# Performance work log

Measured on AMD Instinct MI355X. Metric: run time of the kernel, lower is better.

## Reference

```python
import jax, jax.numpy as jnp
import numpy as np

N = 100000   # total nodes in batched graph
E = 320000   # total edges
B = 128      # number of graphs in batch
D_IN = 128
H = 256
OUT = 10
L = 4        # num_layers - 1 conv layers
EPS = 1e-6


def setup_inputs() -> dict:
    key = jax.random.key(0)
    ks = jax.random.split(key, 8)
    h = jax.random.normal(ks[0], (N, D_IN), dtype=jnp.float32)
    src = jax.random.randint(ks[1], (E,), 0, N)
    dst = jax.random.randint(ks[2], (E,), 0, N)
    batch_ids = jnp.sort(jax.random.randint(ks[3], (N,), 0, B))
    s = 0.05
    W_first = jax.random.normal(ks[4], (D_IN, H), dtype=jnp.float32) * s
    b_first = jnp.zeros((H,), jnp.float32)
    W_rest = jax.random.normal(ks[5], (L - 1, H, H), dtype=jnp.float32) * s
    b_rest = jnp.zeros((L - 1, H), jnp.float32)
    gamma = jnp.ones((L, H), jnp.float32)
    beta = jnp.zeros((L, H), jnp.float32)
    mean_scale = jnp.ones((L, H), jnp.float32)
    W_pred = jax.random.normal(ks[6], (H, OUT), dtype=jnp.float32) * s
    b_pred = jnp.zeros((OUT,), jnp.float32)
    return dict(h=h, src=src, dst=dst, batch_ids=batch_ids,
                W_first=W_first, b_first=b_first, W_rest=W_rest, b_rest=b_rest,
                gamma=gamma, beta=beta, mean_scale=mean_scale,
                W_pred=W_pred, b_pred=b_pred)


def _graph_conv(h, W, b, src, dst, dinv_src, dinv_dst):
    # DGL GraphConv, norm='both': D_dst^{-1/2} A D_src^{-1/2} h W + b
    x = h * dinv_src[:, None]
    m = jax.ops.segment_sum(x[src], dst, num_segments=N)
    m = m * dinv_dst[:, None]
    return m @ W + b


def _graph_norm(h, gamma, beta, ms, batch_ids, counts):
    # GraphNorm: per-graph mean (scaled by learnable mean_scale) and std
    mean = jax.ops.segment_sum(h, batch_ids, num_segments=B) / counts[:, None]
    sub = h - mean[batch_ids] * ms
    var = jax.ops.segment_sum(sub * sub, batch_ids, num_segments=B) / counts[:, None]
    inv_std = jax.lax.rsqrt(var + EPS)
    return gamma * sub * inv_std[batch_ids] + beta


def reference(h, src, dst, batch_ids, W_first, b_first, W_rest, b_rest,
              gamma, beta, mean_scale, W_pred, b_pred):
    ones_e = jnp.ones((E,), h.dtype)
    deg_out = jnp.maximum(jax.ops.segment_sum(ones_e, src, num_segments=N), 1.0)
    deg_in = jnp.maximum(jax.ops.segment_sum(ones_e, dst, num_segments=N), 1.0)
    dinv_src = jax.lax.rsqrt(deg_out)
    dinv_dst = jax.lax.rsqrt(deg_in)
    counts = jnp.maximum(
        jax.ops.segment_sum(jnp.ones((N,), h.dtype), batch_ids, num_segments=B), 1.0)

    for i in range(L):
        x = h
        if i == 0:
            h = _graph_conv(h, W_first, b_first, src, dst, dinv_src, dinv_dst)
        else:
            h = _graph_conv(h, W_rest[i - 1], b_rest[i - 1], src, dst, dinv_src, dinv_dst)
        h = _graph_norm(h, gamma[i], beta[i], mean_scale[i], batch_ids, counts)
        if i != 0:
            h = jax.nn.relu(h) + x
        else:
            h = jax.nn.relu(h)

    pooled = jax.ops.segment_sum(h, batch_ids, num_segments=B)  # [B, H]
    # dropout is identity at eval
    return pooled @ W_pred + b_pred
```

## Files before the change

### kernel.cpp

```cpp
#include <hip/hip_runtime.h>

#define N_NODES 100000
#define N_PAD   100096
#define N_EDGES 320000
#define NB      128
#define DIN     128
#define H       256
#define OUT_DIM 10
#define EPSV    1e-6f
#define SCAN_B  256
#define PSLICES 32
#define NBLK    (N_PAD / 64)
#define NXCD    8

typedef unsigned short bf16_t;
typedef __attribute__((ext_vector_type(8))) short bf16x8;
typedef __attribute__((ext_vector_type(4))) float f32x4;

__device__ __forceinline__ float bf2f(bf16_t u) {
    union { unsigned int i; float f; } x;
    x.i = ((unsigned int)u) << 16;
    return x.f;
}
__device__ __forceinline__ bf16_t f2bf(float f) {
    union { float f; unsigned int i; } x;
    x.f = f;
    unsigned int r = x.i + 0x7fffu + ((x.i >> 16) & 1u);
    return (bf16_t)(r >> 16);
}

__device__ __forceinline__ int xcd_swz(int bid, int nwg) {
    int q = nwg / NXCD, r = nwg % NXCD;
    int x = bid % NXCD, j = bid / NXCD;
    int base = (x < r) ? x * (q + 1) : r * (q + 1) + (x - r) * q;
    return base + j;
}

__global__ void k_edge_deg(const int* __restrict__ src, const int* __restrict__ dst,
                           int* deg) {
    int e = blockIdx.x * blockDim.x + threadIdx.x;
    if (e < N_EDGES) {
        atomicAdd(&deg[src[e]], 1);
        atomicAdd(&deg[N_NODES + dst[e]], 1);
    }
}

__global__ void k_gstart_relpk(const int* __restrict__ bid, int* __restrict__ gstart,
                               float* __restrict__ countsf, unsigned int* __restrict__ relpk) {
    if (blockIdx.x == 0) {
        int b = threadIdx.x;
        if (b <= NB) {
            int lo = 0, hi = N_NODES;
            while (lo < hi) {
                int mid = (lo + hi) >> 1;
                if (bid[mid] < b) lo = mid + 1; else hi = mid;
            }
            gstart[b] = lo;
        }
        __syncthreads();
        if (b < NB) countsf[b] = (float)max(gstart[b + 1] - gstart[b], 1);
    }
    int idx = blockIdx.x * blockDim.x + threadIdx.x;
    if (idx >= NBLK * 16) return;
    int t = idx >> 4, w = idx & 15;
    int row0 = t * 64;
    int g0 = bid[(row0 < N_NODES) ? row0 : (N_NODES - 1)];
    unsigned int pk = 0;
    for (int j = 0; j < 4; ++j) {
        int r = row0 + w * 4 + j;
        unsigned int rel = 255u;
        if (r < N_NODES) {
            int d = bid[r] - g0;
            rel = (d >= 0 && d < 255) ? (unsigned int)d : 255u;
        }
        pk |= rel << (8 * j);
    }
    relpk[idx] = pk;
}

__global__ void k_scan1(const int* __restrict__ deg_in, int* incl, int* bsums) {
    __shared__ int s[SCAN_B];
    int i = blockIdx.x * SCAN_B + threadIdx.x;
    int v = (i < N_NODES) ? deg_in[i] : 0;
    s[threadIdx.x] = v;
    __syncthreads();
    for (int d = 1; d < SCAN_B; d <<= 1) {
        int t = (threadIdx.x >= d) ? s[threadIdx.x - d] : 0;
        __syncthreads();
        s[threadIdx.x] += t;
        __syncthreads();
    }
    if (i < N_NODES) incl[i] = s[threadIdx.x];
    if (threadIdx.x == SCAN_B - 1) bsums[blockIdx.x] = s[threadIdx.x];
}

__global__ void k_scan2(const int* __restrict__ bsums, int* boffs, int nb) {
    __shared__ int s[512];
    int t = threadIdx.x;
    int v = (t < nb) ? bsums[t] : 0;
    s[t] = v;
    __syncthreads();
    for (int d = 1; d < 512; d <<= 1) {
        int x = (t >= d) ? s[t - d] : 0;
        __syncthreads();
        s[t] += x;
        __syncthreads();
    }
    if (t < nb) boffs[t] = s[t] - v;
}

__global__ void k_scan3(const int* __restrict__ deg, const int* __restrict__ incl,
                        const int* __restrict__ boffs, int* row_start, int* cursor,
                        float* dinv_src, float* dinv_dst) {
    int i = blockIdx.x * blockDim.x + threadIdx.x;
    if (i < N_NODES) {
        int ex = incl[i] - deg[N_NODES + i] + boffs[i / SCAN_B];
        row_start[i] = ex;
        cursor[i]    = ex;
        dinv_src[i] = rsqrtf((float)max(deg[i], 1));
        dinv_dst[i] = rsqrtf((float)max(deg[N_NODES + i], 1));
    }
    if (i == 0) row_start[N_NODES] = N_EDGES;
}

__global__ void k_scatter(const int* __restrict__ src, const int* __restrict__ dst,
                          int* cursor, int* csr_src) {
    int e = blockIdx.x * blockDim.x + threadIdx.x;
    if (e < N_EDGES) {
        int slot = atomicAdd(&cursor[dst[e]], 1);
        csr_src[slot] = src[e];
    }
}

__global__ void k_wt(const float* __restrict__ Wf, const float* __restrict__ Wr,
                     bf16_t* __restrict__ Wt0, bf16_t* __restrict__ Wt123) {
    int idx = blockIdx.x * 256 + threadIdx.x;
    if (idx < H * DIN) {
        int c = idx / DIN, k = idx % DIN;
        Wt0[idx] = f2bf(Wf[k * H + c]);
        return;
    }
    idx -= H * DIN;
    if (idx >= 3 * H * H) return;
    int l = idx / (H * H);
    int rem = idx % (H * H);
    int c = rem / H, k = rem % H;
    Wt123[idx] = f2bf(Wr[(size_t)l * H * H + k * H + c]);
}

__global__ void k_prescale(const float* __restrict__ h, const float* __restrict__ dinv_s,
                           bf16_t* __restrict__ hs) {
    int idx = xcd_swz(blockIdx.x, 12500) * 256 + threadIdx.x;
    if (idx >= N_NODES * (DIN / 4)) return;
    int n = idx >> 5;
    float w = dinv_s[n];
    float4 v = reinterpret_cast<const float4*>(h)[idx];
    ushort4 o;
    o.x = f2bf(v.x * w); o.y = f2bf(v.y * w);
    o.z = f2bf(v.z * w); o.w = f2bf(v.w * w);
    reinterpret_cast<ushort4*>(hs)[idx] = o;
}

template <int NC, bool PS>
__global__ void k_agg(const bf16_t* __restrict__ hx, const float* __restrict__ dinv_s,
                      const float* __restrict__ dinv_d, const int* __restrict__ row_start,
                      const int* __restrict__ csr_src, bf16_t* __restrict__ m) {
    constexpr int VEC = NC / 64;
    int gid  = xcd_swz(blockIdx.x, 25000) * blockDim.x + threadIdx.x;
    int v    = gid >> 6;
    int lane = gid & 63;
    if (v >= N_NODES) return;
    float acc[VEC] = {};
    int s0 = row_start[v], s1 = row_start[v + 1];

    auto body = [&](int ei) {
        int si = csr_src[ei];
        float wv = 1.f;
        if constexpr (!PS) wv = dinv_s[si];
        if constexpr (VEC == 4) {
            ushort4 r = *reinterpret_cast<const ushort4*>(hx + (size_t)si * NC + lane * 4);
            acc[0] += bf2f(r.x) * wv; acc[1] += bf2f(r.y) * wv;
            acc[2] += bf2f(r.z) * wv; acc[3] += bf2f(r.w) * wv;
        } else {
            ushort2 r = *reinterpret_cast<const ushort2*>(hx + (size_t)si * NC + lane * 2);
            acc[0] += bf2f(r.x) * wv; acc[1] += bf2f(r.y) * wv;
        }
    };

    int e = s0;
    for (; e + 3 < s1; e += 4) { body(e); body(e + 1); body(e + 2); body(e + 3); }
    for (; e < s1; ++e) body(e);

    float wd = dinv_d[v];
    if constexpr (VEC == 4) {
        ushort4 o;
        o.x = f2bf(acc[0] * wd); o.y = f2bf(acc[1] * wd);
        o.z = f2bf(acc[2] * wd); o.w = f2bf(acc[3] * wd);
        *reinterpret_cast<ushort4*>(m + (size_t)v * NC + lane * 4) = o;
    } else {
        ushort2 o; o.x = f2bf(acc[0] * wd); o.y = f2bf(acc[1] * wd);
        *reinterpret_cast<ushort2*>(m + (size_t)v * NC + lane * 2) = o;
    }
}

template <int K>
__global__ __launch_bounds__(256, 2) void k_gemm_mfma(const bf16_t* __restrict__ A,
                                                      const bf16_t* __restrict__ Wt,
                                                      const float* __restrict__ bias,
                                                      const unsigned int* __restrict__ relpk,
                                                      bf16_t* __restrict__ C,
                                                      float2* __restrict__ part) {
    __shared__ bf16_t lds_raw[64 * (H + 8)];
    constexpr int LKA = K + 8;
    bf16_t (*aT)[LKA] = reinterpret_cast<bf16_t (*)[LKA]>(lds_raw);
    bf16_t (*cT)[H + 8] = reinterpret_cast<bf16_t (*)[H + 8]>(lds_raw);
    constexpr int KS = K / 32;

    const int tid  = threadIdx.x;
    const int wave = tid >> 6;
    const int lane = tid & 63;
    const int pb   = xcd_swz(blockIdx.x, NBLK);
    const int row0 = pb * 64;
    const int col0 = wave * 64;
    const int lr = lane & 15;
    const int lg = lane >> 4;

    const bf16_t* Bb = Wt + (size_t)(col0 + lr) * K + lg * 8;
    bf16x8 ball[KS][4];
    #pragma unroll
    for (int ks = 0; ks < KS; ++ks)
        #pragma unroll
        for (int nt = 0; nt < 4; ++nt)
            ball[ks][nt] = *reinterpret_cast<const bf16x8*>(Bb + (size_t)nt * 16 * K + ks * 32);

    {
        const bf16_t* Ag = A + (size_t)row0 * K;
        constexpr int CHUNKS = 64 * K / 8;
        #pragma unroll
        for (int it = 0; it < CHUNKS / 256; ++it) {
            int ci  = it * 256 + tid;
            int row = (ci * 8) / K;
            int col = (ci * 8) % K;
            uint4 v = *reinterpret_cast<const uint4*>(Ag + ci * 8);
            *reinterpret_cast<uint4*>(&aT[row][col]) = v;
        }
    }
    __syncthreads();

    f32x4 acc[4][4] = {};

    #pragma unroll
    for (int ks = 0; ks < KS; ++ks) {
        bf16x8 a[4];
        #pragma unroll
        for (int mt = 0; mt < 4; ++mt)
            a[mt] = *reinterpret_cast<const bf16x8*>(&aT[mt * 16 + lr][ks * 32 + lg * 8]);
        #pragma unroll
        for (int mt = 0; mt < 4; ++mt)
            #pragma unroll
            for (int nt = 0; nt < 4; ++nt)
                acc[mt][nt] = __builtin_amdgcn_mfma_f32_16x16x32_bf16(a[mt], ball[ks][nt], acc[mt][nt], 0, 0, 0);
    }

    float bsn[4];
    #pragma unroll
    for (int nt = 0; nt < 4; ++nt) bsn[nt] = bias[col0 + nt * 16 + lr];

    {
        unsigned int relw[4];
        #pragma unroll
        for (int mt = 0; mt < 4; ++mt)
            relw[mt] = relpk[pb * 16 + mt * 4 + lg];

        float sA[3][4] = {}, qA[3][4] = {};
        #pragma unroll
        for (int mt = 0; mt < 4; ++mt) {
            #pragma unroll
            for (int j = 0; j < 4; ++j) {
                int rv = (relw[mt] >> (8 * j)) & 0xff;
                #pragma unroll
                for (int nt = 0; nt < 4; ++nt) {
                    float v  = acc[mt][nt][j] + bsn[nt];
                    float v0 = (rv == 0) ? v : 0.f;
                    float v1 = (rv == 1) ? v : 0.f;
                    float v2 = (rv == 2) ? v : 0.f;
                    sA[0][nt] += v0; qA[0][nt] += v0 * v0;
                    sA[1][nt] += v1; qA[1][nt] += v1 * v1;
                    sA[2][nt] += v2; qA[2][nt] += v2 * v2;
                }
            }
        }
        #pragma unroll
        for (int rel = 0; rel < 3; ++rel) {
            #pragma unroll
            for (int nt = 0; nt < 4; ++nt) {
                float sv = sA[rel][nt], qv = qA[rel][nt];
                sv += __shfl_xor(sv, 16); qv += __shfl_xor(qv, 16);
                sv += __shfl_xor(sv, 32); qv += __shfl_xor(qv, 32);
                sA[rel][nt] = sv; qA[rel][nt] = qv;
            }
        }
        if (lg == 0) {
            constexpr size_t PLANE = (size_t)NBLK * H;
            #pragma unroll
            for (int rel = 0; rel < 3; ++rel)
                #pragma unroll
                for (int nt = 0; nt < 4; ++nt)
                    part[(size_t)rel * PLANE + (size_t)pb * H + col0 + nt * 16 + lr]
                        = make_float2(sA[rel][nt], qA[rel][nt]);
        }
    }

    __syncthreads();

    #pragma unroll
    for (int nt = 0; nt < 4; ++nt) {
        int c = col0 + nt * 16 + lr;
        #pragma unroll
        for (int mt = 0; mt < 4; ++mt) {
            #pragma unroll
            for (int j = 0; j < 4; ++j)
                cT[mt * 16 + lg * 4 + j][c] = f2bf(acc[mt][nt][j] + bsn[nt]);
        }
    }
    __syncthreads();

    #pragma unroll
    for (int it = 0; it < 8; ++it) {
        int i = it * 256 + tid;
        int r = i >> 5;
        int s = i & 31;
        *reinterpret_cast<uint4*>(C + (size_t)(row0 + r) * H + s * 8) =
            *reinterpret_cast<const uint4*>(&cT[r][s * 8]);
    }
}

__global__ void k_stats_red(const float2* __restrict__ part, const int* __restrict__ bid,
                            const int* __restrict__ gstart, const float* __restrict__ countsf,
                            const float* __restrict__ gamma, const float* __restrict__ beta,
                            const float* __restrict__ msc,
                            float* __restrict__ scale, float* __restrict__ shift) {
    constexpr size_t PLANE = (size_t)NBLK * H;
    int b = blockIdx.x;
    int c = threadIdx.x;
    int n0 = gstart[b], n1 = gstart[b + 1];
    float s = 0.f, q = 0.f;
    if (n1 > n0) {
        int blo = n0 >> 6, bhi = (n1 - 1) >> 6;
        for (int blk = blo; blk <= bhi; ++blk) {
            int rel = b - bid[blk << 6];
            if (rel >= 0 && rel < 3) {
                float2 v = part[(size_t)rel * PLANE + (size_t)blk * H + c];
                s += v.x; q += v.y;
            }
        }
    }
    float rc   = 1.0f / countsf[b];
    float mean = s * rc, ex2 = q * rc;
    float mm   = mean * msc[c];
    float var  = ex2 - 2.f * mean * mm + mm * mm;
    float a    = gamma[c] * rsqrtf(var + EPSV);
    scale[b * H + c] = a;
    shift[b * H + c] = beta[c] - a * mm;
}

template <bool RES>
__global__ void k_norm(const bf16_t* __restrict__ y, const bf16_t* __restrict__ resid,
                       const int* __restrict__ bid, const float* __restrict__ scale,
                       const float* __restrict__ shift, bf16_t* __restrict__ outp) {
    int idx = xcd_swz(blockIdx.x, 25000) * 256 + threadIdx.x;
    if (idx >= N_NODES * (H / 4)) return;
    int n  = idx >> 6;
    int f4 = idx & 63;
    int b  = bid[n];
    float4 sc = reinterpret_cast<const float4*>(scale)[b * 64 + f4];
    float4 sh = reinterpret_cast<const float4*>(shift)[b * 64 + f4];
    ushort4 yv = reinterpret_cast<const ushort4*>(y)[idx];
    float o0 = fmaxf(bf2f(yv.x) * sc.x + sh.x, 0.f);
    float o1 = fmaxf(bf2f(yv.y) * sc.y + sh.y, 0.f);
    float o2 = fmaxf(bf2f(yv.z) * sc.z + sh.z, 0.f);
    float o3 = fmaxf(bf2f(yv.w) * sc.w + sh.w, 0.f);
    if constexpr (RES) {
        ushort4 r = reinterpret_cast<const ushort4*>(resid)[idx];
        o0 += bf2f(r.x); o1 += bf2f(r.y); o2 += bf2f(r.z); o3 += bf2f(r.w);
    }
    ushort4 o;
    o.x = f2bf(o0); o.y = f2bf(o1); o.z = f2bf(o2); o.w = f2bf(o3);
    reinterpret_cast<ushort4*>(outp)[idx] = o;
}

__global__ void k_pool(const bf16_t* __restrict__ hf, const int* __restrict__ gstart,
                       float* __restrict__ pp) {
    int b = blockIdx.x, sl = blockIdx.y, f = threadIdx.x;
    int n0 = gstart[b], n1 = gstart[b + 1];
    int cnt = n1 - n0;
    int lo = n0 + (int)((long long)cnt * sl / PSLICES);
    int hi = n0 + (int)((long long)cnt * (sl + 1) / PSLICES);
    float s = 0.f;
    for (int n = lo; n < hi; ++n) s += bf2f(hf[(size_t)n * H + f]);
    pp[((size_t)b * PSLICES + sl) * H + f] = s;
}

__global__ void k_pred(const float* __restrict__ pp, const float* __restrict__ Wp,
                       const float* __restrict__ bp, float* __restrict__ outp) {
    __shared__ float row[H];
    int b = blockIdx.x, f = threadIdx.x;
    float s = 0.f;
    for (int sl = 0; sl < PSLICES; ++sl)
        s += pp[((size_t)b * PSLICES + sl) * H + f];
    row[f] = s;
    __syncthreads();
    if (f < OUT_DIM) {
        float acc = bp[f];
        for (int k = 0; k < H; ++k) acc += row[k] * Wp[k * OUT_DIM + f];
        outp[b * OUT_DIM + f] = acc;
    }
}

extern "C" void kernel_launch(void* const* d_in, const int* in_sizes, int n_in,
                              void* d_out, int out_size, void* d_ws, size_t ws_size,
                              hipStream_t stream) {
    const float* h_in  = (const float*)d_in[0];
    const int*   src   = (const int*)d_in[1];
    const int*   dst   = (const int*)d_in[2];
    const int*   bid   = (const int*)d_in[3];
    const float* Wf    = (const float*)d_in[4];
    const float* bfv   = (const float*)d_in[5];
    const float* Wr    = (const float*)d_in[6];
    const float* br    = (const float*)d_in[7];
    const float* gamma = (const float*)d_in[8];
    const float* beta  = (const float*)d_in[9];
    const float* ms    = (const float*)d_in[10];
    const float* Wp    = (const float*)d_in[11];
    const float* bp    = (const float*)d_in[12];
    float* outp = (float*)d_out;

    char* w = (char*)d_ws;
    size_t off = 0;
    auto alloc = [&](size_t bytes) -> void* {
        void* p = w + off;
        off = (off + bytes + 255) & ~(size_t)255;
        return p;
    };
    bf16_t* bufA = (bf16_t*)alloc((size_t)N_PAD * H * 2);
    bf16_t* bufB = (bf16_t*)alloc((size_t)N_PAD * H * 2);
    bf16_t* bufC = (bf16_t*)alloc((size_t)N_PAD * H * 2);
    bf16_t* Wt0  = (bf16_t*)alloc((size_t)H * DIN * 2);
    bf16_t* Wt123= (bf16_t*)alloc((size_t)3 * H * H * 2);
    int* deg       = (int*)alloc((size_t)2 * N_NODES * 4);
    float* dinv_src = (float*)alloc(N_NODES * 4);
    float* dinv_dst = (float*)alloc(N_NODES * 4);
    int* incl_tmp  = (int*)alloc(N_NODES * 4);
    int* bsums     = (int*)alloc(512 * 4);
    int* boffs     = (int*)alloc(512 * 4);
    int* row_start = (int*)alloc((N_NODES + 1) * 4);
    int* cursor    = (int*)alloc(N_NODES * 4);
    int* csr_src   = (int*)alloc(N_EDGES * 4);
    int* gstart    = (int*)alloc((NB + 1) * 4);
    float* countsf = (float*)alloc(NB * 4);
    float* gscale  = (float*)alloc((size_t)NB * H * 4);
    float* gshift  = (float*)alloc((size_t)NB * H * 4);
    float2* part   = (float2*)alloc((size_t)3 * NBLK * H * 8);
    unsigned int* relpk = (unsigned int*)alloc((size_t)NBLK * 16 * 4);
    float* pp      = (float*)alloc((size_t)NB * PSLICES * H * 4);

    if (off > ws_size) return;

    bf16_t* hs = bufB;

    const int nscan = (N_NODES + SCAN_B - 1) / SCAN_B;

    hipMemsetAsync(deg, 0, (size_t)2 * N_NODES * 4, stream);

    k_edge_deg<<<(N_EDGES + 255) / 256, 256, 0, stream>>>(src, dst, deg);
    k_gstart_relpk<<<(NBLK * 16 + 255) / 256, 256, 0, stream>>>(bid, gstart, countsf, relpk);
    k_scan1<<<nscan, SCAN_B, 0, stream>>>(deg + N_NODES, incl_tmp, bsums);
    k_scan2<<<1, 512, 0, stream>>>(bsums, boffs, nscan);
    k_scan3<<<(N_NODES + 255) / 256, 256, 0, stream>>>(deg, incl_tmp, boffs, row_start, cursor,
                                                       dinv_src, dinv_dst);
    k_scatter<<<(N_EDGES + 255) / 256, 256, 0, stream>>>(src, dst, cursor, csr_src);
    k_wt<<<(H * DIN + 3 * H * H + 255) / 256, 256, 0, stream>>>(Wf, Wr, Wt0, Wt123);

    const int aggGrid  = (N_NODES + 3) / 4;
    const int normGrid = (N_NODES * (H / 4) + 255) / 256;

    k_prescale<<<(N_NODES * (DIN / 4) + 255) / 256, 256, 0, stream>>>(h_in, dinv_src, hs);
    k_agg<DIN, true><<<aggGrid, 256, 0, stream>>>(hs, nullptr, dinv_dst, row_start, csr_src, bufA);
    k_gemm_mfma<DIN><<<NBLK, 256, 0, stream>>>(bufA, Wt0, bfv, relpk, bufB, part);
    k_stats_red<<<NB, H, 0, stream>>>(part, bid, gstart, countsf, gamma, beta, ms,
                                      gscale, gshift);
    k_norm<false><<<normGrid, 256, 0, stream>>>(bufB, nullptr, bid, gscale, gshift, bufC);

    bf16_t* hx = bufC;
    bf16_t* f1 = bufA;
    bf16_t* f2 = bufB;
    for (int i = 1; i < 4; ++i) {
        k_agg<H, false><<<aggGrid, 256, 0, stream>>>(hx, dinv_src, dinv_dst, row_start, csr_src, f1);
        k_gemm_mfma<H><<<NBLK, 256, 0, stream>>>(f1, Wt123 + (size_t)(i - 1) * H * H,
                                                 br + (i - 1) * H, relpk, f2, part);
        k_stats_red<<<NB, H, 0, stream>>>(part, bid, gstart, countsf, gamma + i * H,
                                          beta + i * H, ms + i * H, gscale, gshift);
        k_norm<true><<<normGrid, 256, 0, stream>>>(f2, hx, bid, gscale, gshift, f1);
        bf16_t* nh = f1; f1 = hx; hx = nh;
    }

    k_pool<<<dim3(NB, PSLICES), H, 0, stream>>>(hx, gstart, pp);
    k_pred<<<NB, H, 0, stream>>>(pp, Wp, bp, outp);
}
```

Baseline: 561.4 us.

## Fuse neighbor aggregation into MFMA GEMM and drop prescale kernel

Merges the CSR gather-aggregation kernel into the GEMM kernel: each 64-row block aggregates its rows' neighbors directly into LDS as bf16, then runs the MFMA product, and layer 0 reads fp32 input with per-edge dinv_src instead of a separate prescale pass. This removes the intermediate aggregated-matrix write/read and two launches per layer. It changes parallelism: 4 threads per row, each serially walking all edges with 32-wide accumulators, so gathers are less coalesced and register pressure rises. B fragments are now loaded per k-step instead of all at once.

Measured after the change: 570.4 us. About the same (+1.6%).

```diff
diff --git a/kernel.cpp b/kernel.cpp
--- a/kernel.cpp
+++ b/kernel.cpp
@@ -15,6 +15,7 @@
 
 typedef unsigned short bf16_t;
 typedef __attribute__((ext_vector_type(8))) short bf16x8;
+typedef __attribute__((ext_vector_type(8))) unsigned short ushort8_t;
 typedef __attribute__((ext_vector_type(4))) float f32x4;
 
 __device__ __forceinline__ float bf2f(bf16_t u) {
@@ -148,68 +149,17 @@
     Wt123[idx] = f2bf(Wr[(size_t)l * H * H + k * H + c]);
 }
 
-__global__ void k_prescale(const float* __restrict__ h, const float* __restrict__ dinv_s,
-                           bf16_t* __restrict__ hs) {
-    int idx = xcd_swz(blockIdx.x, 12500) * 256 + threadIdx.x;
-    if (idx >= N_NODES * (DIN / 4)) return;
-    int n = idx >> 5;
-    float w = dinv_s[n];
-    float4 v = reinterpret_cast<const float4*>(h)[idx];
-    ushort4 o;
-    o.x = f2bf(v.x * w); o.y = f2bf(v.y * w);
-    o.z = f2bf(v.z * w); o.w = f2bf(v.w * w);
-    reinterpret_cast<ushort4*>(hs)[idx] = o;
-}
-
-template <int NC, bool PS>
-__global__ void k_agg(const bf16_t* __restrict__ hx, const float* __restrict__ dinv_s,
-                      const float* __restrict__ dinv_d, const int* __restrict__ row_start,
-                      const int* __restrict__ csr_src, bf16_t* __restrict__ m) {
-    constexpr int VEC = NC / 64;
-    int gid  = xcd_swz(blockIdx.x, 25000) * blockDim.x + threadIdx.x;
-    int v    = gid >> 6;
-    int lane = gid & 63;
-    if (v >= N_NODES) return;
-    float acc[VEC] = {};
-    int s0 = row_start[v], s1 = row_start[v + 1];
-
-    auto body = [&](int ei) {
-        int si = csr_src[ei];
-        float wv = 1.f;
-        if constexpr (!PS) wv = dinv_s[si];
-        if constexpr (VEC == 4) {
-            ushort4 r = *reinterpret_cast<const ushort4*>(hx + (size_t)si * NC + lane * 4);
-            acc[0] += bf2f(r.x) * wv; acc[1] += bf2f(r.y) * wv;
-            acc[2] += bf2f(r.z) * wv; acc[3] += bf2f(r.w) * wv;
-        } else {
-            ushort2 r = *reinterpret_cast<const ushort2*>(hx + (size_t)si * NC + lane * 2);
-            acc[0] += bf2f(r.x) * wv; acc[1] += bf2f(r.y) * wv;
-        }
-    };
-
-    int e = s0;
-    for (; e + 3 < s1; e += 4) { body(e); body(e + 1); body(e + 2); body(e + 3); }
-    for (; e < s1; ++e) body(e);
-
-    float wd = dinv_d[v];
-    if constexpr (VEC == 4) {
-        ushort4 o;
-        o.x = f2bf(acc[0] * wd); o.y = f2bf(acc[1] * wd);
-        o.z = f2bf(acc[2] * wd); o.w = f2bf(acc[3] * wd);
-        *reinterpret_cast<ushort4*>(m + (size_t)v * NC + lane * 4) = o;
-    } else {
-        ushort2 o; o.x = f2bf(acc[0] * wd); o.y = f2bf(acc[1] * wd);
-        *reinterpret_cast<ushort2*>(m + (size_t)v * NC + lane * 2) = o;
-    }
-}
-
-template <int K>
-__global__ __launch_bounds__(256, 2) void k_gemm_mfma(const bf16_t* __restrict__ A,
-                                                      const bf16_t* __restrict__ Wt,
-                                                      const float* __restrict__ bias,
-                                                      const unsigned int* __restrict__ relpk,
-                                                      bf16_t* __restrict__ C,
-                                                      float2* __restrict__ part) {
+template <int K, bool L0>
+__global__ __launch_bounds__(256, 2) void k_aggemm(const void* __restrict__ hxv,
+                                                   const float* __restrict__ dinv_s,
+                                                   const float* __restrict__ dinv_d,
+                                                   const int* __restrict__ row_start,
+                                                   const int* __restrict__ csr_src,
+                                                   const bf16_t* __restrict__ Wt,
+                                                   const float* __restrict__ bias,
+                                                   const unsigned int* __restrict__ relpk,
+                                                   bf16_t* __restrict__ C,
+                                                   float2* __restrict__ part) {
     __shared__ bf16_t lds_raw[64 * (H + 8)];
     constexpr int LKA = K + 8;
     bf16_t (*aT)[LKA] = reinterpret_cast<bf16_t (*)[LKA]>(lds_raw);
@@ -225,41 +175,71 @@
     const int lr = lane & 15;
     const int lg = lane >> 4;
 
+    {
+        const int rr = tid >> 2;
+        const int r  = row0 + rr;
+        const int ch = tid & 3;
+        int s0 = 0, s1 = 0;
+        float wd = 0.f;
+        if (r < N_NODES) { s0 = row_start[r]; s1 = row_start[r + 1]; wd = dinv_d[r]; }
+        constexpr int CPT = K / 4;
+        constexpr int HALVES = CPT / 32;
+        #pragma unroll
+        for (int hf = 0; hf < HALVES; ++hf) {
+            const int cbase = ch * CPT + hf * 32;
+            float fa[32] = {};
+            for (int e = s0; e < s1; ++e) {
+                int si = csr_src[e];
+                float wv = dinv_s[si];
+                if constexpr (L0) {
+                    const float* p = (const float*)hxv + (size_t)si * K + cbase;
+                    #pragma unroll
+                    for (int j = 0; j < 8; ++j) {
+                        float4 v = reinterpret_cast<const float4*>(p)[j];
+                        fa[4 * j + 0] += v.x * wv; fa[4 * j + 1] += v.y * wv;
+                        fa[4 * j + 2] += v.z * wv; fa[4 * j + 3] += v.w * wv;
+                    }
+                } else {
+                    const bf16_t* p = (const bf16_t*)hxv + (size_t)si * K + cbase;
+                    #pragma unroll
+                    for (int j = 0; j < 4; ++j) {
+                        ushort8_t v = *reinterpret_cast<const ushort8_t*>(p + 8 * j);
+                        fa[8 * j + 0] += bf2f(v[0]) * wv; fa[8 * j + 1] += bf2f(v[1]) * wv;
+                        fa[8 * j + 2] += bf2f(v[2]) * wv; fa[8 * j + 3] += bf2f(v[3]) * wv;
+                        fa[8 * j + 4] += bf2f(v[4]) * wv; fa[8 * j + 5] += bf2f(v[5]) * wv;
+                        fa[8 * j + 6] += bf2f(v[6]) * wv; fa[8 * j + 7] += bf2f(v[7]) * wv;
+                    }
+                }
+            }
+            #pragma unroll
+            for (int j = 0; j < 8; ++j) {
+                ushort4 o;
+                o.x = f2bf(fa[4 * j + 0] * wd); o.y = f2bf(fa[4 * j + 1] * wd);
+                o.z = f2bf(fa[4 * j + 2] * wd); o.w = f2bf(fa[4 * j + 3] * wd);
+                *reinterpret_cast<ushort4*>(&aT[rr][cbase + 4 * j]) = o;
+            }
+        }
+    }
+    __syncthreads();
+
+    f32x4 acc[4][4] = {};
+
     const bf16_t* Bb = Wt + (size_t)(col0 + lr) * K + lg * 8;
-    bf16x8 ball[KS][4];
-    #pragma unroll
-    for (int ks = 0; ks < KS; ++ks)
-        #pragma unroll
-        for (int nt = 0; nt < 4; ++nt)
-            ball[ks][nt] = *reinterpret_cast<const bf16x8*>(Bb + (size_t)nt * 16 * K + ks * 32);
-
-    {
-        const bf16_t* Ag = A + (size_t)row0 * K;
-        constexpr int CHUNKS = 64 * K / 8;
-        #pragma unroll
-        for (int it = 0; it < CHUNKS / 256; ++it) {
-            int ci  = it * 256 + tid;
-            int row = (ci * 8) / K;
-            int col = (ci * 8) % K;
-            uint4 v = *reinterpret_cast<const uint4*>(Ag + ci * 8);
-            *reinterpret_cast<uint4*>(&aT[row][col]) = v;
-        }
-    }
-    __syncthreads();
-
-    f32x4 acc[4][4] = {};
 
     #pragma unroll
     for (int ks = 0; ks < KS; ++ks) {
-        bf16x8 a[4];
+        bf16x8 a[4], b[4];
         #pragma unroll
         for (int mt = 0; mt < 4; ++mt)
             a[mt] = *reinterpret_cast<const bf16x8*>(&aT[mt * 16 + lr][ks * 32 + lg * 8]);
         #pragma unroll
+        for (int nt = 0; nt < 4; ++nt)
+            b[nt] = *reinterpret_cast<const bf16x8*>(Bb + (size_t)nt * 16 * K + ks * 32);
+        #pragma unroll
         for (int mt = 0; mt < 4; ++mt)
             #pragma unroll
             for (int nt = 0; nt < 4; ++nt)
-                acc[mt][nt] = __builtin_amdgcn_mfma_f32_16x16x32_bf16(a[mt], ball[ks][nt], acc[mt][nt], 0, 0, 0);
+                acc[mt][nt] = __builtin_amdgcn_mfma_f32_16x16x32_bf16(a[mt], b[nt], acc[mt][nt], 0, 0, 0);
     }
 
     float bsn[4];
@@ -466,8 +446,6 @@
 
     if (off > ws_size) return;
 
-    bf16_t* hs = bufB;
-
     const int nscan = (N_NODES + SCAN_B - 1) / SCAN_B;
 
     hipMemsetAsync(deg, 0, (size_t)2 * N_NODES * 4, stream);
@@ -481,26 +459,23 @@
     k_scatter<<<(N_EDGES + 255) / 256, 256, 0, stream>>>(src, dst, cursor, csr_src);
     k_wt<<<(H * DIN + 3 * H * H + 255) / 256, 256, 0, stream>>>(Wf, Wr, Wt0, Wt123);
 
-    const int aggGrid  = (N_NODES + 3) / 4;
     const int normGrid = (N_NODES * (H / 4) + 255) / 256;
 
-    k_prescale<<<(N_NODES * (DIN / 4) + 255) / 256, 256, 0, stream>>>(h_in, dinv_src, hs);
-    k_agg<DIN, true><<<aggGrid, 256, 0, stream>>>(hs, nullptr, dinv_dst, row_start, csr_src, bufA);
-    k_gemm_mfma<DIN><<<NBLK, 256, 0, stream>>>(bufA, Wt0, bfv, relpk, bufB, part);
+    k_aggemm<DIN, true><<<NBLK, 256, 0, stream>>>(h_in, dinv_src, dinv_dst, row_start,
+                                                  csr_src, Wt0, bfv, relpk, bufB, part);
     k_stats_red<<<NB, H, 0, stream>>>(part, bid, gstart, countsf, gamma, beta, ms,
                                       gscale, gshift);
     k_norm<false><<<normGrid, 256, 0, stream>>>(bufB, nullptr, bid, gscale, gshift, bufC);
 
     bf16_t* hx = bufC;
     bf16_t* f1 = bufA;
-    bf16_t* f2 = bufB;
     for (int i = 1; i < 4; ++i) {
-        k_agg<H, false><<<aggGrid, 256, 0, stream>>>(hx, dinv_src, dinv_dst, row_start, csr_src, f1);
-        k_gemm_mfma<H><<<NBLK, 256, 0, stream>>>(f1, Wt123 + (size_t)(i - 1) * H * H,
-                                                 br + (i - 1) * H, relpk, f2, part);
+        k_aggemm<H, false><<<NBLK, 256, 0, stream>>>(hx, dinv_src, dinv_dst, row_start,
+                                                     csr_src, Wt123 + (size_t)(i - 1) * H * H,
+                                                     br + (i - 1) * H, relpk, bufB, part);
         k_stats_red<<<NB, H, 0, stream>>>(part, bid, gstart, countsf, gamma + i * H,
                                           beta + i * H, ms + i * H, gscale, gshift);
-        k_norm<true><<<normGrid, 256, 0, stream>>>(f2, hx, bid, gscale, gshift, f1);
+        k_norm<true><<<normGrid, 256, 0, stream>>>(bufB, hx, bid, gscale, gshift, f1);
         bf16_t* nh = f1; f1 = hx; hx = nh;
     }
 
```
